# Kernel tuning notes

Measured on AMD Instinct MI355X. Metric: run time of the kernel, lower is better.

The kernel has to match this reference:

```python
import jax, jax.numpy as jnp
import numpy as np

BS, C_IN, CTX, TGT = 2, 8, 1024, 96
D_MODEL, N_HEADS, D_FF, N_LAYERS = 256, 16, 1024, 4
PF, SF, PC, SC = 8, 4, 32, 16
NF = (CTX + SF - PF) // SF + 1   # 256 fine patches (incl. end-pad)
NC = (CTX + SC - PC) // SC + 1   # 64 coarse patches
TOTAL = NF + NC                  # 320
EPS = 1e-5
DK = D_MODEL // N_HEADS
SCALE = DK ** -0.5


def _patchify(z, plen, stride):
    # ReplicationPad1d((0, stride)) then unfold -> (bs, c, n_patches, plen)
    pad = jnp.broadcast_to(z[..., -1:], z.shape[:-1] + (stride,))
    zp = jnp.concatenate([z, pad], axis=-1)
    n = (zp.shape[-1] - plen) // stride + 1
    idx = np.arange(n)[:, None] * stride + np.arange(plen)[None, :]
    return zp[..., idx]


def _layernorm(x, s, b):
    m = x.mean(-1, keepdims=True)
    v = jnp.var(x, axis=-1, keepdims=True)
    return (x - m) * jax.lax.rsqrt(v + EPS) * s + b


def setup_inputs() -> dict:
    key = jax.random.key(0)
    ks = jax.random.split(key, 16)
    g = lambda k, shape: jax.random.normal(k, shape, jnp.float32) * 0.02
    return {
        "z": jax.random.normal(ks[0], (BS, C_IN, CTX), jnp.float32),
        "revin_w": jnp.ones((C_IN,), jnp.float32),
        "revin_b": jnp.zeros((C_IN,), jnp.float32),
        "Wf": g(ks[1], (PF, D_MODEL)), "bf": jnp.zeros((D_MODEL,), jnp.float32),
        "Wc": g(ks[2], (PC, D_MODEL)), "bc": jnp.zeros((D_MODEL,), jnp.float32),
        "W_pos": jax.random.uniform(ks[3], (TOTAL, D_MODEL), jnp.float32, -0.02, 0.02),
        "WQ": g(ks[4], (N_LAYERS, D_MODEL, D_MODEL)), "bQ": jnp.zeros((N_LAYERS, D_MODEL), jnp.float32),
        "WK": g(ks[5], (N_LAYERS, D_MODEL, D_MODEL)), "bK": jnp.zeros((N_LAYERS, D_MODEL), jnp.float32),
        "WV": g(ks[6], (N_LAYERS, D_MODEL, D_MODEL)), "bV": jnp.zeros((N_LAYERS, D_MODEL), jnp.float32),
        "WO": g(ks[7], (N_LAYERS, D_MODEL, D_MODEL)), "bO": jnp.zeros((N_LAYERS, D_MODEL), jnp.float32),
        "ln1_s": jnp.ones((N_LAYERS, D_MODEL), jnp.float32), "ln1_b": jnp.zeros((N_LAYERS, D_MODEL), jnp.float32),
        "ln2_s": jnp.ones((N_LAYERS, D_MODEL), jnp.float32), "ln2_b": jnp.zeros((N_LAYERS, D_MODEL), jnp.float32),
        "F1": g(ks[8], (N_LAYERS, D_MODEL, D_FF)), "c1": jnp.zeros((N_LAYERS, D_FF), jnp.float32),
        "F2": g(ks[9], (N_LAYERS, D_FF, D_MODEL)), "c2": jnp.zeros((N_LAYERS, D_MODEL), jnp.float32),
        "Wh": g(ks[10], (D_MODEL * TOTAL, TGT)), "bh": jnp.zeros((TGT,), jnp.float32),
    }


def reference(z, revin_w, revin_b, Wf, bf, Wc, bc, W_pos, WQ, bQ, WK, bK, WV, bV,
              WO, bO, ln1_s, ln1_b, ln2_s, ln2_b, F1, c1, F2, c2, Wh, bh):
    # RevIN norm over the time axis (last axis of (bs, c, T))
    mean = z.mean(-1, keepdims=True)
    std = jnp.sqrt(jnp.var(z, axis=-1, keepdims=True) + EPS)
    zn = (z - mean) / std * revin_w[None, :, None] + revin_b[None, :, None]

    # dual-scale patch embedding
    x_fine = _patchify(zn, PF, SF) @ Wf + bf      # (bs, c, NF, d)
    x_coarse = _patchify(zn, PC, SC) @ Wc + bc    # (bs, c, NC, d)
    x = jnp.concatenate([x_fine, x_coarse], axis=2)  # (bs, c, TOTAL, d)

    u = x.reshape(BS * C_IN, TOTAL, D_MODEL) + W_pos  # (B, S, d), B=bs*c

    # residual-score transformer encoder (post-norm)
    prev = None
    for l in range(N_LAYERS):
        q = (u @ WQ[l] + bQ[l]).reshape(-1, TOTAL, N_HEADS, DK).transpose(0, 2, 1, 3)
        k = (u @ WK[l] + bK[l]).reshape(-1, TOTAL, N_HEADS, DK).transpose(0, 2, 1, 3)
        v = (u @ WV[l] + bV[l]).reshape(-1, TOTAL, N_HEADS, DK).transpose(0, 2, 1, 3)
        s = jnp.einsum('bhqd,bhkd->bhqk', q, k) * SCALE
        if prev is not None:
            s = s + prev
        w = jax.nn.softmax(s, axis=-1)
        o = jnp.einsum('bhqk,bhkd->bhqd', w, v).transpose(0, 2, 1, 3).reshape(-1, TOTAL, D_MODEL)
        o = o @ WO[l] + bO[l]
        u = _layernorm(u + o, ln1_s[l], ln1_b[l])
        h = jax.nn.gelu(u @ F1[l] + c1[l], approximate=False) @ F2[l] + c2[l]
        u = _layernorm(u + h, ln2_s[l], ln2_b[l])
        prev = s

    # head: (bs, c, TOTAL, d) -> permute -> flatten(d, TOTAL) -> linear
    zz = u.reshape(BS, C_IN, TOTAL, D_MODEL).transpose(0, 1, 3, 2).reshape(BS, C_IN, D_MODEL * TOTAL)
    out = zz @ Wh + bh  # (bs, c, TGT)

    # RevIN denorm
    out = (out - revin_b[None, :, None]) / (revin_w[None, :, None] + EPS * EPS) * std + mean
    return out
```

## Files before the change

### kernel.cpp

```cpp
#include <hip/hip_runtime.h>
#include <math.h>

typedef unsigned short ushort;
typedef unsigned int uint;
typedef __attribute__((ext_vector_type(8))) short short8;
typedef __attribute__((ext_vector_type(4))) float f32x4;
typedef __attribute__((ext_vector_type(4))) ushort us4;

constexpr int BS = 2, C_IN = 8, CTX = 1024, TGT = 96;
constexpr int DM = 256, NH = 16, DFF = 1024, NL = 4;
constexpr int NF = 256, TOTAL = 320;
constexpr int NB = 16;
constexpr int DK = 16;
constexpr float EPS = 1e-5f;
constexpr float SCALE = 0.25f;
constexpr int KHEAD = DM * TOTAL;
constexpr int M = NB * TOTAL;

__device__ __forceinline__ ushort f2b(float x) {
    uint u = __float_as_uint(x);
    u += 0x7fff + ((u >> 16) & 1);
    return (ushort)(u >> 16);
}
__device__ __forceinline__ float bu2f(ushort x) { return __uint_as_float(((uint)x) << 16); }
__device__ __forceinline__ uint pack2(float a, float b) { return (uint)f2b(a) | ((uint)f2b(b) << 16); }

typedef __attribute__((address_space(3))) uint lds_u32;
typedef const __attribute__((address_space(1))) uint glb_u32;
__device__ __forceinline__ void ldst16(const void* g, void* l) {
    __builtin_amdgcn_global_load_lds((glb_u32*)g, (lds_u32*)l, 16, 0, 0);
}

#define PIPE_BARRIER() asm volatile("s_waitcnt vmcnt(0)\n\ts_barrier" ::: "memory")

__global__ __launch_bounds__(256) void k_prep(
        const float* __restrict__ WQ, const float* __restrict__ WK,
        const float* __restrict__ WV, const float* __restrict__ WO,
        const float* __restrict__ F1, const float* __restrict__ F2,
        const float* __restrict__ Wh,
        ushort* __restrict__ Wtqkv, ushort* __restrict__ WtO,
        ushort* __restrict__ Ft1, ushort* __restrict__ Ft2,
        ushort* __restrict__ WhT2,
        const float* __restrict__ z, const float* __restrict__ rw,
        const float* __restrict__ rb,
        const float* __restrict__ Wf, const float* __restrict__ bfv,
        const float* __restrict__ Wc, const float* __restrict__ bcv,
        const float* __restrict__ Wpos, ushort* __restrict__ u,
        const float* __restrict__ bhv, float* __restrict__ outp,
        float* __restrict__ scalef) {
    __shared__ __align__(16) ushort tile[64 * 98];
    __shared__ float szn[CTX];
    __shared__ float red1[4], red2[4];
    int i = blockIdx.x, tid = threadIdx.x;

    if (i < 768) {
        const float* src; ushort* dst; int lsrc, ldst_, r0, c0;
        if (i < 256) {
            int mat = i >> 4, l = mat >> 2, w = mat & 3;
            src = (w == 0 ? WQ : (w == 1 ? WK : (w == 2 ? WV : WO))) + l * 65536;
            dst = (w < 3) ? (Wtqkv + (size_t)l * 768 * 256 + w * 65536)
                          : (WtO + (size_t)l * 65536);
            lsrc = 256; ldst_ = 256; r0 = ((i >> 2) & 3) * 64; c0 = (i & 3) * 64;
        } else if (i < 512) {
            int j = i - 256, l = j >> 6, t = j & 63;
            src = F1 + (size_t)l * 262144; dst = Ft1 + (size_t)l * 262144;
            lsrc = 1024; ldst_ = 256; r0 = (t >> 4) * 64; c0 = (t & 15) * 64;
        } else {
            int j = i - 512, l = j >> 6, t = j & 63;
            src = F2 + (size_t)l * 262144; dst = Ft2 + (size_t)l * 262144;
            lsrc = 256; ldst_ = 1024; r0 = (t >> 2) * 64; c0 = (t & 3) * 64;
        }
#pragma unroll
        for (int it = 0; it < 4; it++) {
            int fid = it * 256 + tid;
            int fr = fid >> 4, fc = fid & 15;
            f32x4 v = *(const f32x4*)&src[(size_t)(r0 + fr) * lsrc + c0 + fc * 4];
            ushort* tr = &tile[fr * 66];
            tr[fc * 4 + 0] = f2b(v[0]); tr[fc * 4 + 1] = f2b(v[1]);
            tr[fc * 4 + 2] = f2b(v[2]); tr[fc * 4 + 3] = f2b(v[3]);
        }
        __syncthreads();
#pragma unroll
        for (int it = 0; it < 4; it++) {
            int sid = it * 256 + tid;
            int cr = sid >> 4, cc = sid & 15;
            us4 v = (us4){ tile[(cc * 4 + 0) * 66 + cr], tile[(cc * 4 + 1) * 66 + cr],
                           tile[(cc * 4 + 2) * 66 + cr], tile[(cc * 4 + 3) * 66 + cr] };
            *(us4*)&dst[(size_t)(c0 + cr) * ldst_ + r0 + cc * 4] = v;
        }
    } else if (i < 2048) {
        int j = i - 768;
        int pp = j >> 2, d0 = (j & 3) * 64;
#pragma unroll
        for (int it = 0; it < 6; it++) {
            int fid = it * 256 + tid;
            int fr = fid / 24, fc = fid % 24;
            f32x4 v = *(const f32x4*)&Wh[((size_t)(d0 + fr) * 320 + pp) * 96 + fc * 4];
            ushort* tr = &tile[fr * 98];
            tr[fc * 4 + 0] = f2b(v[0]); tr[fc * 4 + 1] = f2b(v[1]);
            tr[fc * 4 + 2] = f2b(v[2]); tr[fc * 4 + 3] = f2b(v[3]);
        }
        __syncthreads();
#pragma unroll
        for (int it = 0; it < 6; it++) {
            int sid = it * 256 + tid;
            int tr = sid >> 4, dc = sid & 15;
            us4 v = (us4){ tile[(dc * 4 + 0) * 98 + tr], tile[(dc * 4 + 1) * 98 + tr],
                           tile[(dc * 4 + 2) * 98 + tr], tile[(dc * 4 + 3) * 98 + tr] };
            *(us4*)&WhT2[(size_t)tr * KHEAD + pp * 256 + d0 + dc * 4] = v;
        }
    } else {
        int j = i - 2048;
        int bc = j / 80, pb = j % 80;
        int wave = tid >> 6, lane = tid & 63;
        f32x4 zv = *(const f32x4*)&z[bc * CTX + tid * 4];
        float s1 = zv[0] + zv[1] + zv[2] + zv[3];
        float s2 = zv[0] * zv[0] + zv[1] * zv[1] + zv[2] * zv[2] + zv[3] * zv[3];
#pragma unroll
        for (int off = 1; off < 64; off <<= 1) {
            s1 += __shfl_xor(s1, off);
            s2 += __shfl_xor(s2, off);
        }
        if (lane == 0) { red1[wave] = s1; red2[wave] = s2; }
        __syncthreads();
        s1 = red1[0] + red1[1] + red1[2] + red1[3];
        s2 = red2[0] + red2[1] + red2[2] + red2[3];
        float m = s1 * (1.0f / CTX);
        float var = s2 * (1.0f / CTX) - m * m;
        float sd = sqrtf(var + EPS);
        int c = bc & 7;
        float w = rw[c], bb = rb[c];
        float inv_sd_w = w / sd;
#pragma unroll
        for (int k = 0; k < 4; k++) szn[tid * 4 + k] = (zv[k] - m) * inv_sd_w + bb;
        if (pb == 0) {
            if (tid < TGT) outp[bc * TGT + tid] = (bhv[tid] - bb) / (w + EPS * EPS) * sd + m;
            if (tid == 0) scalef[bc] = sd / (w + EPS * EPS);
        }
        __syncthreads();
#pragma unroll
        for (int pi = 0; pi < 4; pi++) {
            int p = pb * 4 + pi, d = tid;
            float acc;
            if (p < NF) {
                acc = bfv[d];
                int base = p * 4;
#pragma unroll
                for (int q = 0; q < 8; q++)
                    acc += szn[min(base + q, CTX - 1)] * Wf[q * DM + d];
            } else {
                acc = bcv[d];
                int base = (p - NF) * 16;
#pragma unroll
                for (int q = 0; q < 32; q++)
                    acc += szn[min(base + q, CTX - 1)] * Wc[q * DM + d];
            }
            acc += Wpos[p * DM + d];
            u[((size_t)bc * TOTAL + p) * DM + d] = f2b(acc);
        }
    }
}

template <int GELU, int QKV>
__global__ __launch_bounds__(256) void k_gemm_mfma(const ushort* __restrict__ A,
                                                   const ushort* __restrict__ Wt,
                                                   const float* __restrict__ b0,
                                                   const float* __restrict__ b1,
                                                   const float* __restrict__ b2,
                                                   ushort* __restrict__ C,
                                                   ushort* __restrict__ C2,
                                                   int Mm, int N, int K) {
    __shared__ ushort As[2][64][32];
    __shared__ ushort Bs[2][64][32];
    int tid = threadIdx.x;
    int wave = tid >> 6, lane = tid & 63;
    int quad = lane >> 4, l16 = lane & 15;
    int m0 = blockIdx.y * 64, n0 = blockIdx.x * 64;

    f32x4 acc[4];
#pragma unroll
    for (int nt = 0; nt < 4; nt++) acc[nt] = (f32x4){0.f, 0.f, 0.f, 0.f};

    int srow = wave * 16 + (lane >> 2);
    int sc = (lane & 3) ^ ((srow >> 1) & 3);
    const ushort* Ag = &A[(size_t)(m0 + srow) * K + sc * 8];
    const ushort* Bg = &Wt[(size_t)(n0 + srow) * K + sc * 8];
    int rchunk = (quad ^ ((l16 >> 1) & 3)) * 8;

    ldst16(Ag, &As[0][wave * 16][0]);
    ldst16(Bg, &Bs[0][wave * 16][0]);
    PIPE_BARRIER();

    int nstep = K >> 5;
    int cur = 0;
    for (int t = 0; t < nstep; t++) {
        if (t + 1 < nstep) {
            ldst16(Ag + (t + 1) * 32, &As[cur ^ 1][wave * 16][0]);
            ldst16(Bg + (t + 1) * 32, &Bs[cur ^ 1][wave * 16][0]);
        }
        short8 af = *(const short8*)&As[cur][wave * 16 + l16][rchunk];
#pragma unroll
        for (int nt = 0; nt < 4; nt++) {
            short8 bf = *(const short8*)&Bs[cur][nt * 16 + l16][rchunk];
            acc[nt] = __builtin_amdgcn_mfma_f32_16x16x32_bf16(af, bf, acc[nt], 0, 0, 0);
        }
        PIPE_BARRIER();
        cur ^= 1;
    }
#pragma unroll
    for (int nt = 0; nt < 4; nt++) {
        int col = n0 + nt * 16 + l16;
        float bi;
        if (QKV) {
            int bs = (n0 + nt * 16) >> 8;
            const float* bp = bs == 0 ? b0 : (bs == 1 ? b1 : b2);
            bi = bp[col & 255];
        } else {
            bi = b0[col];
        }
#pragma unroll
        for (int r = 0; r < 4; r++) {
            int rowm = m0 + wave * 16 + quad * 4 + r;
            float vv = acc[nt][r] + bi;
            if (GELU) vv = vv * 0.5f * (1.0f + erff(vv * 0.70710678118f));
            if (QKV) {
                int bs = col >> 8;
                int c = col & 255, hh = c >> 4, d = c & 15;
                int bb = rowm / 320, j = rowm - bb * 320;
                size_t plane = (size_t)hh * (M * DK) + (size_t)bb * (TOTAL * DK);
                if (bs == 0) {
                    C[plane + (size_t)j * DK + d] = f2b(vv);
                } else if (bs == 1) {
                    int off = (((j >> 4) * 2 + (d >> 3)) * 16 + (j & 15)) * 8 + (d & 7);
                    C[(size_t)M * DM + plane + off] = f2b(vv);
                } else {
                    int off = ((j >> 5) * 4 + ((j & 15) >> 2)) * 128 +
                              (((j >> 4) & 1) << 2) + (j & 3) + d * 8;
                    C2[plane + off] = f2b(vv);
                }
            } else {
                C[(size_t)rowm * N + col] = f2b(vv);
            }
        }
    }
}

__global__ __launch_bounds__(256) void k_gemm_ln16(const ushort* __restrict__ A,
                                                   const ushort* __restrict__ Wt,
                                                   const float* __restrict__ bias,
                                                   const float* __restrict__ ls,
                                                   const float* __restrict__ lb,
                                                   ushort* __restrict__ u, int K) {
    __shared__ ushort As[2][16][32];
    __shared__ ushort Bs[2][256][32];
    __shared__ float ps1[16][4], ps2[16][4];
    int tid = threadIdx.x;
    int wave = tid >> 6, lane = tid & 63;
    int quad = lane >> 4, l16 = lane & 15;
    int m0 = blockIdx.x * 16;

    f32x4 acc[4];
#pragma unroll
    for (int nt = 0; nt < 4; nt++) acc[nt] = (f32x4){0.f, 0.f, 0.f, 0.f};

    int brow = wave * 16 + (lane >> 2);
    int bc_swz = (lane & 3) ^ ((brow >> 1) & 3);
    const ushort* Bg0 = &Wt[(size_t)brow * K + bc_swz * 8];
    int ar = lane >> 2;
    int ac = (lane & 3) ^ ((ar >> 1) & 3);
    const ushort* Ag = &A[(size_t)(m0 + ar) * K + ac * 8];
    int rchunk = (quad ^ ((l16 >> 1) & 3)) * 8;

    if (tid < 64) ldst16(Ag, &As[0][0][0]);
#pragma unroll
    for (int i = 0; i < 4; i++)
        ldst16(Bg0 + (size_t)i * 64 * K, &Bs[0][i * 64 + wave * 16][0]);
    PIPE_BARRIER();

    int nstep = K >> 5;
    int cur = 0;
    for (int t = 0; t < nstep; t++) {
        if (t + 1 < nstep) {
            if (tid < 64) ldst16(Ag + (t + 1) * 32, &As[cur ^ 1][0][0]);
#pragma unroll
            for (int i = 0; i < 4; i++)
                ldst16(Bg0 + (size_t)i * 64 * K + (t + 1) * 32, &Bs[cur ^ 1][i * 64 + wave * 16][0]);
        }
        short8 af = *(const short8*)&As[cur][l16][rchunk];
#pragma unroll
        for (int nt = 0; nt < 4; nt++) {
            short8 bf = *(const short8*)&Bs[cur][wave * 64 + nt * 16 + l16][rchunk];
            acc[nt] = __builtin_amdgcn_mfma_f32_16x16x32_bf16(af, bf, acc[nt], 0, 0, 0);
        }
        PIPE_BARRIER();
        cur ^= 1;
    }
    float xv[4][4];
#pragma unroll
    for (int r = 0; r < 4; r++) {
        int rowg = m0 + quad * 4 + r;
        float s1 = 0.f, s2 = 0.f;
#pragma unroll
        for (int nt = 0; nt < 4; nt++) {
            int col = wave * 64 + nt * 16 + l16;
            float x = acc[nt][r] + bias[col] + bu2f(u[(size_t)rowg * DM + col]);
            xv[r][nt] = x; s1 += x; s2 += x * x;
        }
        s1 += __shfl_xor(s1, 1); s2 += __shfl_xor(s2, 1);
        s1 += __shfl_xor(s1, 2); s2 += __shfl_xor(s2, 2);
        s1 += __shfl_xor(s1, 4); s2 += __shfl_xor(s2, 4);
        s1 += __shfl_xor(s1, 8); s2 += __shfl_xor(s2, 8);
        if (l16 == 0) { ps1[quad * 4 + r][wave] = s1; ps2[quad * 4 + r][wave] = s2; }
    }
    __syncthreads();
#pragma unroll
    for (int r = 0; r < 4; r++) {
        int rowl = quad * 4 + r, rowg = m0 + rowl;
        float s1 = ps1[rowl][0] + ps1[rowl][1] + ps1[rowl][2] + ps1[rowl][3];
        float s2 = ps2[rowl][0] + ps2[rowl][1] + ps2[rowl][2] + ps2[rowl][3];
        float m = s1 * (1.0f / DM);
        float var = s2 * (1.0f / DM) - m * m;
        float rs = rsqrtf(var + EPS);
#pragma unroll
        for (int nt = 0; nt < 4; nt++) {
            int col = wave * 64 + nt * 16 + l16;
            u[(size_t)rowg * DM + col] = f2b((xv[r][nt] - m) * rs * ls[col] + lb[col]);
        }
    }
}

__global__ __launch_bounds__(256, 3) void k_attn(const ushort* __restrict__ qk, const ushort* __restrict__ vm,
                                                 ushort* __restrict__ ao, int nj) {
    __shared__ __align__(16) ushort sh[25600];
    int bh = blockIdx.x, b = bh >> 4, h = bh & 15;
    int i0 = blockIdx.y * 64;
    int t = threadIdx.x, wave = t >> 6, lane = t & 63, quad = lane >> 4, l16 = lane & 15;
    const short8 zero8 = (short8){0, 0, 0, 0, 0, 0, 0, 0};
    size_t hplane = (size_t)h * (M * DK) + (size_t)b * (TOTAL * DK);

    int nchunks = (nj + 1) * 10;
    for (int c = wave; c < nchunks; c += 4) {
        int s = c / 10, cc = c - s * 10;
        const ushort* src = (s < nj)
            ? qk + (size_t)(2 * s + 1) * (M * DM) + hplane + cc * 512
            : vm + hplane + cc * 512;
        int dstbase = (s < nj ? s * 5120 : 20480) + cc * 512;
        ldst16(src + lane * 8, &sh[dstbase]);
    }
    short8 qfr[4] = { zero8, zero8, zero8, zero8 };
    int qrow = i0 + wave * 16 + l16;
#pragma unroll
    for (int jl = 0; jl < 4; jl++)
        if (jl < nj && quad < 2)
            qfr[jl] = *(const short8*)&qk[(size_t)(2 * jl) * (M * DM) + hplane +
                                          (size_t)qrow * DK + quad * 8];
    PIPE_BARRIER();

    f32x4 acc[20];
#pragma unroll
    for (int nt = 0; nt < 20; nt++) acc[nt] = (f32x4){0.f, 0.f, 0.f, 0.f};

    __builtin_amdgcn_s_setprio(1);
#pragma unroll
    for (int jl = 0; jl < 4; jl++) {
        if (jl < nj) {
            int kb = jl * 5120;
#pragma unroll
            for (int nt = 0; nt < 20; nt++) {
                short8 kf = *(const short8*)&sh[kb + ((nt * 2 + (quad & 1)) * 16 + l16) * 8];
                acc[nt] = __builtin_amdgcn_mfma_f32_16x16x32_bf16(kf, qfr[jl], acc[nt], 0, 0, 0);
            }
        }
    }
    __builtin_amdgcn_s_setprio(0);

    float mx = -1e30f;
#pragma unroll
    for (int nt = 0; nt < 20; nt++)
#pragma unroll
        for (int r = 0; r < 4; r++) { acc[nt][r] *= SCALE; mx = fmaxf(mx, acc[nt][r]); }
    mx = fmaxf(mx, __shfl_xor(mx, 16));
    mx = fmaxf(mx, __shfl_xor(mx, 32));
    float sum = 0.f;
#pragma unroll
    for (int nt = 0; nt < 20; nt++)
#pragma unroll
        for (int r = 0; r < 4; r++) { acc[nt][r] = __expf(acc[nt][r] - mx); sum += acc[nt][r]; }
    sum += __shfl_xor(sum, 16);
    sum += __shfl_xor(sum, 32);
    float inv = 1.f / sum;
#pragma unroll
    for (int nt = 0; nt < 20; nt++)
#pragma unroll
        for (int r = 0; r < 4; r++) acc[nt][r] *= inv;

    f32x4 oacc = (f32x4){0.f, 0.f, 0.f, 0.f};
    __builtin_amdgcn_s_setprio(1);
#pragma unroll
    for (int jt2 = 0; jt2 < 10; jt2++) {
        short8 vt = *(const short8*)&sh[20480 + ((jt2 * 4 + quad) * 16 + l16) * 8];
        union { short8 v; uint u[4]; } pf;
        pf.u[0] = pack2(acc[2 * jt2][0], acc[2 * jt2][1]);
        pf.u[1] = pack2(acc[2 * jt2][2], acc[2 * jt2][3]);
        pf.u[2] = pack2(acc[2 * jt2 + 1][0], acc[2 * jt2 + 1][1]);
        pf.u[3] = pack2(acc[2 * jt2 + 1][2], acc[2 * jt2 + 1][3]);
        oacc = __builtin_amdgcn_mfma_f32_16x16x32_bf16(vt, pf.v, oacc, 0, 0, 0);
    }
    __builtin_amdgcn_s_setprio(0);
    us4 ov4 = (us4){f2b(oacc[0]), f2b(oacc[1]), f2b(oacc[2]), f2b(oacc[3])};
    *(us4*)&ao[((size_t)b * TOTAL + i0 + wave * 16 + l16) * DM + h * DK + quad * 4] = ov4;
}

__global__ __launch_bounds__(256) void k_head(const ushort* __restrict__ u, const ushort* __restrict__ WhT2,
                                              const float* __restrict__ scalef, float* __restrict__ out) {
    int t0 = blockIdx.x * 16;
    int wave = threadIdx.x >> 6, lane = threadIdx.x & 63;
    int quad = lane >> 4, l16 = lane & 15;
    int chunk = blockIdx.y * 4 + wave;
    int kbeg = chunk * 1024;
    f32x4 acc = (f32x4){0.f, 0.f, 0.f, 0.f};
    const ushort* za = &u[(size_t)l16 * KHEAD + quad * 8];
    const ushort* wb = &WhT2[(size_t)(t0 + l16) * KHEAD + quad * 8];
#pragma unroll 4
    for (int k = kbeg; k < kbeg + 1024; k += 32) {
        short8 af = *(const short8*)&za[k];
        short8 bf = *(const short8*)&wb[k];
        acc = __builtin_amdgcn_mfma_f32_16x16x32_bf16(af, bf, acc, 0, 0, 0);
    }
#pragma unroll
    for (int r = 0; r < 4; r++) {
        int bcr = quad * 4 + r;
        atomicAdd(&out[bcr * TGT + t0 + l16], acc[r] * scalef[bcr]);
    }
}

extern "C" void kernel_launch(void* const* d_in, const int* in_sizes, int n_in,
                              void* d_out, int out_size, void* d_ws, size_t ws_size,
                              hipStream_t stream) {
    const float* z       = (const float*)d_in[0];
    const float* revin_w = (const float*)d_in[1];
    const float* revin_b = (const float*)d_in[2];
    const float* Wf      = (const float*)d_in[3];
    const float* bfv     = (const float*)d_in[4];
    const float* Wc      = (const float*)d_in[5];
    const float* bcv     = (const float*)d_in[6];
    const float* Wpos    = (const float*)d_in[7];
    const float* WQ      = (const float*)d_in[8];
    const float* bQ      = (const float*)d_in[9];
    const float* WK      = (const float*)d_in[10];
    const float* bK      = (const float*)d_in[11];
    const float* WV      = (const float*)d_in[12];
    const float* bV      = (const float*)d_in[13];
    const float* WO      = (const float*)d_in[14];
    const float* bO      = (const float*)d_in[15];
    const float* ln1s    = (const float*)d_in[16];
    const float* ln1b    = (const float*)d_in[17];
    const float* ln2s    = (const float*)d_in[18];
    const float* ln2b    = (const float*)d_in[19];
    const float* F1      = (const float*)d_in[20];
    const float* c1      = (const float*)d_in[21];
    const float* F2      = (const float*)d_in[22];
    const float* c2      = (const float*)d_in[23];
    const float* Wh      = (const float*)d_in[24];
    const float* bh      = (const float*)d_in[25];
    float* out = (float*)d_out;

    char* p = (char*)d_ws;
    float* scalef = (float*)p;   p += 16 * 4;
    p = (char*)(((size_t)p + 255) & ~255ull);
    ushort* u     = (ushort*)p;  p += (size_t)M * DM * 2;
    ushort* qkbuf = (ushort*)p;  p += (size_t)NL * 2 * M * DM * 2;
    ushort* vbuf  = (ushort*)p;  p += (size_t)M * DM * 2;
    ushort* ax    = (ushort*)p;  p += (size_t)M * DM * 2;
    ushort* hbuf  = (ushort*)p;  p += (size_t)M * DFF * 2;
    ushort* Wtqkv = (ushort*)p;  p += (size_t)NL * 768 * 256 * 2;
    ushort* WtO   = (ushort*)p;  p += (size_t)NL * 256 * 256 * 2;
    ushort* Ft1   = (ushort*)p;  p += (size_t)NL * 1024 * 256 * 2;
    ushort* Ft2   = (ushort*)p;  p += (size_t)NL * 256 * 1024 * 2;
    ushort* WhT2  = (ushort*)p;  p += (size_t)TGT * KHEAD * 2;

    k_prep<<<3328, 256, 0, stream>>>(WQ, WK, WV, WO, F1, F2, Wh,
                                     Wtqkv, WtO, Ft1, Ft2, WhT2,
                                     z, revin_w, revin_b,
                                     Wf, bfv, Wc, bcv, Wpos, u,
                                     bh, out, scalef);

    for (int l = 0; l < NL; l++) {
        k_gemm_mfma<0, 1><<<dim3(12, 80), 256, 0, stream>>>(
            u, Wtqkv + (size_t)l * 768 * 256, bQ + l * DM, bK + l * DM, bV + l * DM,
            qkbuf + (size_t)l * 2 * M * DM, vbuf, M, 768, 256);
        k_attn<<<dim3(NB * NH, 5), 256, 0, stream>>>(qkbuf, vbuf, ax, l + 1);
        k_gemm_ln16<<<M / 16, 256, 0, stream>>>(
            ax, WtO + (size_t)l * 65536, bO + l * DM, ln1s + l * DM, ln1b + l * DM, u, 256);
        k_gemm_mfma<1, 0><<<dim3(16, 80), 256, 0, stream>>>(
            u, Ft1 + (size_t)l * 262144, c1 + l * DFF, c1, c1, hbuf, hbuf, M, 1024, 256);
        k_gemm_ln16<<<M / 16, 256, 0, stream>>>(
            hbuf, Ft2 + (size_t)l * 262144, c2 + l * DM, ln2s + l * DM, ln2b + l * DM, u, 1024);
    }

    k_head<<<dim3(TGT / 16, 20), 256, 0, stream>>>(u, WhT2, scalef, out);
}
```

Baseline: 426.1 us.

## Fuse O-proj+LN1, FFN up/GELU/down and LN2 into one per-row-block kernel

Replaces three launches per layer (O-projection with LayerNorm, the FF1 GEMM with GELU, and FF2 with LayerNorm) with a single kernel. Each 16-row block keeps the normalized activations and the GELU intermediate in shared memory and loops over the four 256-wide FF chunks, so the hidden buffer never goes through global memory. The cost is that each block re-streams all of F1/F2 from global/L2 with only 16 rows of reuse, and the grid is limited to 320 blocks doing serial chunk loops.

```diff
diff --git a/kernel.cpp b/kernel.cpp
--- a/kernel.cpp
+++ b/kernel.cpp
@@ -245,72 +245,183 @@
     }
 }
 
-__global__ __launch_bounds__(256) void k_gemm_ln16(const ushort* __restrict__ A,
-                                                   const ushort* __restrict__ Wt,
-                                                   const float* __restrict__ bias,
-                                                   const float* __restrict__ ls,
-                                                   const float* __restrict__ lb,
-                                                   ushort* __restrict__ u, int K) {
+__global__ __launch_bounds__(256) void k_block(const ushort* __restrict__ ax,
+                                               const ushort* __restrict__ WtO,
+                                               const float* __restrict__ bO,
+                                               const float* __restrict__ ln1s,
+                                               const float* __restrict__ ln1b,
+                                               const ushort* __restrict__ F1t,
+                                               const ushort* __restrict__ F2t,
+                                               const float* __restrict__ c1v,
+                                               const float* __restrict__ c2v,
+                                               const float* __restrict__ ln2s,
+                                               const float* __restrict__ ln2b,
+                                               ushort* __restrict__ u) {
     __shared__ ushort As[2][16][32];
     __shared__ ushort Bs[2][256][32];
+    __shared__ __align__(16) ushort Au[16][264];
+    __shared__ __align__(16) ushort Hs[16][264];
     __shared__ float ps1[16][4], ps2[16][4];
     int tid = threadIdx.x;
     int wave = tid >> 6, lane = tid & 63;
     int quad = lane >> 4, l16 = lane & 15;
     int m0 = blockIdx.x * 16;
 
-    f32x4 acc[4];
-#pragma unroll
-    for (int nt = 0; nt < 4; nt++) acc[nt] = (f32x4){0.f, 0.f, 0.f, 0.f};
-
     int brow = wave * 16 + (lane >> 2);
-    int bc_swz = (lane & 3) ^ ((brow >> 1) & 3);
-    const ushort* Bg0 = &Wt[(size_t)brow * K + bc_swz * 8];
+    int bsw = (lane & 3) ^ ((brow >> 1) & 3);
     int ar = lane >> 2;
     int ac = (lane & 3) ^ ((ar >> 1) & 3);
-    const ushort* Ag = &A[(size_t)(m0 + ar) * K + ac * 8];
     int rchunk = (quad ^ ((l16 >> 1) & 3)) * 8;
 
-    if (tid < 64) ldst16(Ag, &As[0][0][0]);
-#pragma unroll
-    for (int i = 0; i < 4; i++)
-        ldst16(Bg0 + (size_t)i * 64 * K, &Bs[0][i * 64 + wave * 16][0]);
-    PIPE_BARRIER();
-
-    int nstep = K >> 5;
-    int cur = 0;
-    for (int t = 0; t < nstep; t++) {
-        if (t + 1 < nstep) {
-            if (tid < 64) ldst16(Ag + (t + 1) * 32, &As[cur ^ 1][0][0]);
-#pragma unroll
-            for (int i = 0; i < 4; i++)
-                ldst16(Bg0 + (size_t)i * 64 * K + (t + 1) * 32, &Bs[cur ^ 1][i * 64 + wave * 16][0]);
-        }
-        short8 af = *(const short8*)&As[cur][l16][rchunk];
+    {
+        f32x4 acc[4];
+#pragma unroll
+        for (int nt = 0; nt < 4; nt++) acc[nt] = (f32x4){0.f, 0.f, 0.f, 0.f};
+        const ushort* Ag = &ax[(size_t)(m0 + ar) * 256 + ac * 8];
+        const ushort* Bg = &WtO[(size_t)brow * 256 + bsw * 8];
+
+        if (tid < 64) ldst16(Ag, &As[0][0][0]);
+#pragma unroll
+        for (int i = 0; i < 4; i++) ldst16(Bg + (size_t)i * 64 * 256, &Bs[0][i * 64 + wave * 16][0]);
+        PIPE_BARRIER();
+        int cur = 0;
+        for (int t = 0; t < 8; t++) {
+            if (t + 1 < 8) {
+                if (tid < 64) ldst16(Ag + (t + 1) * 32, &As[cur ^ 1][0][0]);
+#pragma unroll
+                for (int i = 0; i < 4; i++)
+                    ldst16(Bg + (size_t)i * 64 * 256 + (t + 1) * 32, &Bs[cur ^ 1][i * 64 + wave * 16][0]);
+            }
+            short8 af = *(const short8*)&As[cur][l16][rchunk];
+#pragma unroll
+            for (int nt = 0; nt < 4; nt++) {
+                short8 bf = *(const short8*)&Bs[cur][wave * 64 + nt * 16 + l16][rchunk];
+                acc[nt] = __builtin_amdgcn_mfma_f32_16x16x32_bf16(af, bf, acc[nt], 0, 0, 0);
+            }
+            PIPE_BARRIER();
+            cur ^= 1;
+        }
+        float xv[4][4];
+#pragma unroll
+        for (int r = 0; r < 4; r++) {
+            int rowg = m0 + quad * 4 + r;
+            float s1 = 0.f, s2 = 0.f;
+#pragma unroll
+            for (int nt = 0; nt < 4; nt++) {
+                int col = wave * 64 + nt * 16 + l16;
+                float x = acc[nt][r] + bO[col] + bu2f(u[(size_t)rowg * DM + col]);
+                xv[r][nt] = x; s1 += x; s2 += x * x;
+            }
+            s1 += __shfl_xor(s1, 1); s2 += __shfl_xor(s2, 1);
+            s1 += __shfl_xor(s1, 2); s2 += __shfl_xor(s2, 2);
+            s1 += __shfl_xor(s1, 4); s2 += __shfl_xor(s2, 4);
+            s1 += __shfl_xor(s1, 8); s2 += __shfl_xor(s2, 8);
+            if (l16 == 0) { ps1[quad * 4 + r][wave] = s1; ps2[quad * 4 + r][wave] = s2; }
+        }
+        __syncthreads();
+#pragma unroll
+        for (int r = 0; r < 4; r++) {
+            int rowl = quad * 4 + r;
+            float s1 = ps1[rowl][0] + ps1[rowl][1] + ps1[rowl][2] + ps1[rowl][3];
+            float s2 = ps2[rowl][0] + ps2[rowl][1] + ps2[rowl][2] + ps2[rowl][3];
+            float m = s1 * (1.0f / DM);
+            float var = s2 * (1.0f / DM) - m * m;
+            float rs = rsqrtf(var + EPS);
+#pragma unroll
+            for (int nt = 0; nt < 4; nt++) {
+                int col = wave * 64 + nt * 16 + l16;
+                int k32 = col >> 5, pp = (col >> 3) & 3, e = col & 7;
+                int pphys = pp ^ ((rowl >> 1) & 3);
+                Au[rowl][k32 * 32 + pphys * 8 + e] =
+                    f2b((xv[r][nt] - m) * rs * ln1s[col] + ln1b[col]);
+            }
+        }
+        __syncthreads();
+    }
+
+    f32x4 acc2[4];
+#pragma unroll
+    for (int nt = 0; nt < 4; nt++) acc2[nt] = (f32x4){0.f, 0.f, 0.f, 0.f};
+
+    for (int c = 0; c < 4; c++) {
+        f32x4 acc1[4];
+#pragma unroll
+        for (int nt = 0; nt < 4; nt++) acc1[nt] = (f32x4){0.f, 0.f, 0.f, 0.f};
+        const ushort* Bg1 = &F1t[(size_t)(c * 256 + brow) * 256 + bsw * 8];
+#pragma unroll
+        for (int i = 0; i < 4; i++) ldst16(Bg1 + (size_t)i * 64 * 256, &Bs[0][i * 64 + wave * 16][0]);
+        PIPE_BARRIER();
+        int cur = 0;
+        for (int t = 0; t < 8; t++) {
+            if (t + 1 < 8) {
+#pragma unroll
+                for (int i = 0; i < 4; i++)
+                    ldst16(Bg1 + (size_t)i * 64 * 256 + (t + 1) * 32, &Bs[cur ^ 1][i * 64 + wave * 16][0]);
+            }
+            short8 af = *(const short8*)&Au[l16][t * 32 + rchunk];
+#pragma unroll
+            for (int nt = 0; nt < 4; nt++) {
+                short8 bf = *(const short8*)&Bs[cur][wave * 64 + nt * 16 + l16][rchunk];
+                acc1[nt] = __builtin_amdgcn_mfma_f32_16x16x32_bf16(af, bf, acc1[nt], 0, 0, 0);
+            }
+            PIPE_BARRIER();
+            cur ^= 1;
+        }
 #pragma unroll
         for (int nt = 0; nt < 4; nt++) {
-            short8 bf = *(const short8*)&Bs[cur][wave * 64 + nt * 16 + l16][rchunk];
-            acc[nt] = __builtin_amdgcn_mfma_f32_16x16x32_bf16(af, bf, acc[nt], 0, 0, 0);
-        }
+            int cc = wave * 64 + nt * 16 + l16;
+            float bi = c1v[c * 256 + cc];
+            int k32 = cc >> 5, pp = (cc >> 3) & 3, e = cc & 7;
+#pragma unroll
+            for (int r = 0; r < 4; r++) {
+                int row = quad * 4 + r;
+                float vv = acc1[nt][r] + bi;
+                vv = vv * 0.5f * (1.0f + erff(vv * 0.70710678118f));
+                int pphys = pp ^ ((row >> 1) & 3);
+                Hs[row][k32 * 32 + pphys * 8 + e] = f2b(vv);
+            }
+        }
+        __syncthreads();
+        const ushort* Bg2 = &F2t[(size_t)brow * 1024 + c * 256 + bsw * 8];
+#pragma unroll
+        for (int i = 0; i < 4; i++) ldst16(Bg2 + (size_t)i * 64 * 1024, &Bs[0][i * 64 + wave * 16][0]);
         PIPE_BARRIER();
-        cur ^= 1;
-    }
+        cur = 0;
+        for (int t = 0; t < 8; t++) {
+            if (t + 1 < 8) {
+#pragma unroll
+                for (int i = 0; i < 4; i++)
+                    ldst16(Bg2 + (size_t)i * 64 * 1024 + (t + 1) * 32, &Bs[cur ^ 1][i * 64 + wave * 16][0]);
+            }
+            short8 af = *(const short8*)&Hs[l16][t * 32 + rchunk];
+#pragma unroll
+            for (int nt = 0; nt < 4; nt++) {
+                short8 bf = *(const short8*)&Bs[cur][wave * 64 + nt * 16 + l16][rchunk];
+                acc2[nt] = __builtin_amdgcn_mfma_f32_16x16x32_bf16(af, bf, acc2[nt], 0, 0, 0);
+            }
+            PIPE_BARRIER();
+            cur ^= 1;
+        }
+    }
+
     float xv[4][4];
 #pragma unroll
     for (int r = 0; r < 4; r++) {
-        int rowg = m0 + quad * 4 + r;
+        int rowl = quad * 4 + r;
         float s1 = 0.f, s2 = 0.f;
 #pragma unroll
         for (int nt = 0; nt < 4; nt++) {
             int col = wave * 64 + nt * 16 + l16;
-            float x = acc[nt][r] + bias[col] + bu2f(u[(size_t)rowg * DM + col]);
+            int k32 = col >> 5, pp = (col >> 3) & 3, e = col & 7;
+            int pphys = pp ^ ((rowl >> 1) & 3);
+            float x = acc2[nt][r] + c2v[col] + bu2f(Au[rowl][k32 * 32 + pphys * 8 + e]);
             xv[r][nt] = x; s1 += x; s2 += x * x;
         }
         s1 += __shfl_xor(s1, 1); s2 += __shfl_xor(s2, 1);
         s1 += __shfl_xor(s1, 2); s2 += __shfl_xor(s2, 2);
         s1 += __shfl_xor(s1, 4); s2 += __shfl_xor(s2, 4);
         s1 += __shfl_xor(s1, 8); s2 += __shfl_xor(s2, 8);
-        if (l16 == 0) { ps1[quad * 4 + r][wave] = s1; ps2[quad * 4 + r][wave] = s2; }
+        if (l16 == 0) { ps1[rowl][wave] = s1; ps2[rowl][wave] = s2; }
     }
     __syncthreads();
 #pragma unroll
@@ -324,7 +435,7 @@
 #pragma unroll
         for (int nt = 0; nt < 4; nt++) {
             int col = wave * 64 + nt * 16 + l16;
-            u[(size_t)rowg * DM + col] = f2b((xv[r][nt] - m) * rs * ls[col] + lb[col]);
+            u[(size_t)rowg * DM + col] = f2b((xv[r][nt] - m) * rs * ln2s[col] + ln2b[col]);
         }
     }
 }
@@ -472,7 +583,6 @@
     ushort* qkbuf = (ushort*)p;  p += (size_t)NL * 2 * M * DM * 2;
     ushort* vbuf  = (ushort*)p;  p += (size_t)M * DM * 2;
     ushort* ax    = (ushort*)p;  p += (size_t)M * DM * 2;
-    ushort* hbuf  = (ushort*)p;  p += (size_t)M * DFF * 2;
     ushort* Wtqkv = (ushort*)p;  p += (size_t)NL * 768 * 256 * 2;
     ushort* WtO   = (ushort*)p;  p += (size_t)NL * 256 * 256 * 2;
     ushort* Ft1   = (ushort*)p;  p += (size_t)NL * 1024 * 256 * 2;
@@ -490,12 +600,10 @@
             u, Wtqkv + (size_t)l * 768 * 256, bQ + l * DM, bK + l * DM, bV + l * DM,
             qkbuf + (size_t)l * 2 * M * DM, vbuf, M, 768, 256);
         k_attn<<<dim3(NB * NH, 5), 256, 0, stream>>>(qkbuf, vbuf, ax, l + 1);
-        k_gemm_ln16<<<M / 16, 256, 0, stream>>>(
-            ax, WtO + (size_t)l * 65536, bO + l * DM, ln1s + l * DM, ln1b + l * DM, u, 256);
-        k_gemm_mfma<1, 0><<<dim3(16, 80), 256, 0, stream>>>(
-            u, Ft1 + (size_t)l * 262144, c1 + l * DFF, c1, c1, hbuf, hbuf, M, 1024, 256);
-        k_gemm_ln16<<<M / 16, 256, 0, stream>>>(
-            hbuf, Ft2 + (size_t)l * 262144, c2 + l * DM, ln2s + l * DM, ln2b + l * DM, u, 1024);
+        k_block<<<M / 16, 256, 0, stream>>>(
+            ax, WtO + (size_t)l * 65536, bO + l * DM, ln1s + l * DM, ln1b + l * DM,
+            Ft1 + (size_t)l * 262144, Ft2 + (size_t)l * 262144,
+            c1 + l * DFF, c2 + l * DM, ln2s + l * DM, ln2b + l * DM, u);
     }
 
     k_head<<<dim3(TGT / 16, 20), 256, 0, stream>>>(u, WhT2, scalef, out);
```

After: 419.2 us. About the same (-1.6%).

## Use 128x128-tile GEMM for FFN with split-K partials and separate LN reduction

Applied to the files above, without the earlier changes.

Adds a 128x128 tiled MFMA GEMM used for FF1 with a fused GELU epilogue, and for FF2 as a 4-way split-K that writes fp32 partials. A new kernel then sums the partials, adds bias and the residual, and applies LayerNorm. The 16-row GEMM+LN kernel for FF2 is dropped, which aims to raise tile reuse and parallelism for the K=1024 GEMM. In exchange, the partial buffer costs extra fp32 global traffic and one more kernel launch per layer, and a second u buffer is added so the residual is read separately from the output.

```diff
diff --git a/kernel.cpp b/kernel.cpp
--- a/kernel.cpp
+++ b/kernel.cpp
@@ -245,12 +245,94 @@
     }
 }
 
+template <int GELU, int PART>
+__global__ __launch_bounds__(256) void k_gemm128(const ushort* __restrict__ A,
+                                                 const ushort* __restrict__ Wt,
+                                                 const float* __restrict__ bias,
+                                                 ushort* __restrict__ C,
+                                                 float* __restrict__ Cp,
+                                                 int N, int K, int kc) {
+    __shared__ ushort As[2][128][32];
+    __shared__ ushort Bs[2][128][32];
+    int tid = threadIdx.x;
+    int wave = tid >> 6, lane = tid & 63;
+    int quad = lane >> 4, l16 = lane & 15;
+    int wr = wave >> 1, wc = wave & 1;
+    int m0 = blockIdx.y * 128, n0 = blockIdx.x * 128;
+    int kbeg = blockIdx.z * kc;
+
+    f32x4 acc[4][4];
+#pragma unroll
+    for (int mi = 0; mi < 4; mi++)
+#pragma unroll
+        for (int ni = 0; ni < 4; ni++) acc[mi][ni] = (f32x4){0.f, 0.f, 0.f, 0.f};
+
+    int r4 = lane >> 2;
+    int sc = (lane & 3) ^ ((r4 >> 1) & 3);
+    int srow0 = wave * 32 + r4, srow1 = wave * 32 + 16 + r4;
+    const ushort* Ag0 = &A[(size_t)(m0 + srow0) * K + kbeg + sc * 8];
+    const ushort* Ag1 = &A[(size_t)(m0 + srow1) * K + kbeg + sc * 8];
+    const ushort* Bg0 = &Wt[(size_t)(n0 + srow0) * K + kbeg + sc * 8];
+    const ushort* Bg1 = &Wt[(size_t)(n0 + srow1) * K + kbeg + sc * 8];
+    int rchunk = (quad ^ ((l16 >> 1) & 3)) * 8;
+
+    ldst16(Ag0, &As[0][wave * 32][0]);
+    ldst16(Ag1, &As[0][wave * 32 + 16][0]);
+    ldst16(Bg0, &Bs[0][wave * 32][0]);
+    ldst16(Bg1, &Bs[0][wave * 32 + 16][0]);
+    PIPE_BARRIER();
+
+    int nstep = kc >> 5;
+    int cur = 0;
+    for (int t = 0; t < nstep; t++) {
+        if (t + 1 < nstep) {
+            ldst16(Ag0 + (t + 1) * 32, &As[cur ^ 1][wave * 32][0]);
+            ldst16(Ag1 + (t + 1) * 32, &As[cur ^ 1][wave * 32 + 16][0]);
+            ldst16(Bg0 + (t + 1) * 32, &Bs[cur ^ 1][wave * 32][0]);
+            ldst16(Bg1 + (t + 1) * 32, &Bs[cur ^ 1][wave * 32 + 16][0]);
+        }
+        short8 af[4], bf[4];
+#pragma unroll
+        for (int mi = 0; mi < 4; mi++)
+            af[mi] = *(const short8*)&As[cur][wr * 64 + mi * 16 + l16][rchunk];
+#pragma unroll
+        for (int ni = 0; ni < 4; ni++)
+            bf[ni] = *(const short8*)&Bs[cur][wc * 64 + ni * 16 + l16][rchunk];
+#pragma unroll
+        for (int mi = 0; mi < 4; mi++)
+#pragma unroll
+            for (int ni = 0; ni < 4; ni++)
+                acc[mi][ni] = __builtin_amdgcn_mfma_f32_16x16x32_bf16(af[mi], bf[ni], acc[mi][ni], 0, 0, 0);
+        PIPE_BARRIER();
+        cur ^= 1;
+    }
+
+#pragma unroll
+    for (int mi = 0; mi < 4; mi++)
+#pragma unroll
+        for (int ni = 0; ni < 4; ni++) {
+            int col = n0 + wc * 64 + ni * 16 + l16;
+#pragma unroll
+            for (int r = 0; r < 4; r++) {
+                int row = m0 + wr * 64 + mi * 16 + quad * 4 + r;
+                if (PART) {
+                    Cp[((size_t)blockIdx.z * M + row) * N + col] = acc[mi][ni][r];
+                } else {
+                    float vv = acc[mi][ni][r] + bias[col];
+                    if (GELU) vv = vv * 0.5f * (1.0f + erff(vv * 0.70710678118f));
+                    C[(size_t)row * N + col] = f2b(vv);
+                }
+            }
+        }
+}
+
 __global__ __launch_bounds__(256) void k_gemm_ln16(const ushort* __restrict__ A,
                                                    const ushort* __restrict__ Wt,
                                                    const float* __restrict__ bias,
                                                    const float* __restrict__ ls,
                                                    const float* __restrict__ lb,
-                                                   ushort* __restrict__ u, int K) {
+                                                   const ushort* __restrict__ ures,
+                                                   ushort* __restrict__ uout, int K) {
     __shared__ ushort As[2][16][32];
     __shared__ ushort Bs[2][256][32];
     __shared__ float ps1[16][4], ps2[16][4];
@@ -303,7 +385,7 @@
 #pragma unroll
         for (int nt = 0; nt < 4; nt++) {
             int col = wave * 64 + nt * 16 + l16;
-            float x = acc[nt][r] + bias[col] + bu2f(u[(size_t)rowg * DM + col]);
+            float x = acc[nt][r] + bias[col] + bu2f(ures[(size_t)rowg * DM + col]);
             xv[r][nt] = x; s1 += x; s2 += x * x;
         }
         s1 += __shfl_xor(s1, 1); s2 += __shfl_xor(s2, 1);
@@ -324,8 +406,48 @@
 #pragma unroll
         for (int nt = 0; nt < 4; nt++) {
             int col = wave * 64 + nt * 16 + l16;
-            u[(size_t)rowg * DM + col] = f2b((xv[r][nt] - m) * rs * ls[col] + lb[col]);
-        }
+            uout[(size_t)rowg * DM + col] = f2b((xv[r][nt] - m) * rs * ls[col] + lb[col]);
+        }
+    }
+}
+
+__global__ __launch_bounds__(256) void k_ln2red4(const float* __restrict__ part,
+                                                 const float* __restrict__ c2v,
+                                                 const ushort* __restrict__ u1,
+                                                 const float* __restrict__ ls,
+                                                 const float* __restrict__ lb,
+                                                 ushort* __restrict__ u) {
+    int tid = threadIdx.x;
+    int wave = tid >> 6, lane = tid & 63;
+    int m0 = blockIdx.x * 16;
+#pragma unroll
+    for (int r = 0; r < 4; r++) {
+        int row = m0 + wave * 4 + r;
+        f32x4 a = *(const f32x4*)&part[(size_t)row * 256 + lane * 4];
+        f32x4 b = *(const f32x4*)&part[((size_t)M + row) * 256 + lane * 4];
+        f32x4 c = *(const f32x4*)&part[((size_t)2 * M + row) * 256 + lane * 4];
+        f32x4 d = *(const f32x4*)&part[((size_t)3 * M + row) * 256 + lane * 4];
+        us4 ur = *(const us4*)&u1[(size_t)row * 256 + lane * 4];
+        float x[4];
+        float s1 = 0.f, s2 = 0.f;
+#pragma unroll
+        for (int j = 0; j < 4; j++) {
+            x[j] = a[j] + b[j] + c[j] + d[j] + c2v[lane * 4 + j] + bu2f(ur[j]);
+            s1 += x[j]; s2 += x[j] * x[j];
+        }
+#pragma unroll
+        for (int off = 1; off < 64; off <<= 1) {
+            s1 += __shfl_xor(s1, off);
+            s2 += __shfl_xor(s2, off);
+        }
+        float m = s1 * (1.0f / DM);
+        float var = s2 * (1.0f / DM) - m * m;
+        float rs = rsqrtf(var + EPS);
+        us4 o;
+#pragma unroll
+        for (int j = 0; j < 4; j++)
+            o[j] = f2b((x[j] - m) * rs * ls[lane * 4 + j] + lb[lane * 4 + j]);
+        *(us4*)&u[(size_t)row * 256 + lane * 4] = o;
     }
 }
 
@@ -469,10 +591,12 @@
     float* scalef = (float*)p;   p += 16 * 4;
     p = (char*)(((size_t)p + 255) & ~255ull);
     ushort* u     = (ushort*)p;  p += (size_t)M * DM * 2;
+    ushort* u1    = (ushort*)p;  p += (size_t)M * DM * 2;
     ushort* qkbuf = (ushort*)p;  p += (size_t)NL * 2 * M * DM * 2;
     ushort* vbuf  = (ushort*)p;  p += (size_t)M * DM * 2;
     ushort* ax    = (ushort*)p;  p += (size_t)M * DM * 2;
     ushort* hbuf  = (ushort*)p;  p += (size_t)M * DFF * 2;
+    float* part   = (float*)p;   p += (size_t)4 * M * 256 * 4;
     ushort* Wtqkv = (ushort*)p;  p += (size_t)NL * 768 * 256 * 2;
     ushort* WtO   = (ushort*)p;  p += (size_t)NL * 256 * 256 * 2;
     ushort* Ft1   = (ushort*)p;  p += (size_t)NL * 1024 * 256 * 2;
@@ -491,11 +615,14 @@
             qkbuf + (size_t)l * 2 * M * DM, vbuf, M, 768, 256);
         k_attn<<<dim3(NB * NH, 5), 256, 0, stream>>>(qkbuf, vbuf, ax, l + 1);
         k_gemm_ln16<<<M / 16, 256, 0, stream>>>(
-            ax, WtO + (size_t)l * 65536, bO + l * DM, ln1s + l * DM, ln1b + l * DM, u, 256);
-        k_gemm_mfma<1, 0><<<dim3(16, 80), 256, 0, stream>>>(
-            u, Ft1 + (size_t)l * 262144, c1 + l * DFF, c1, c1, hbuf, hbuf, M, 1024, 256);
-        k_gemm_ln16<<<M / 16, 256, 0, stream>>>(
-            hbuf, Ft2 + (size_t)l * 262144, c2 + l * DM, ln2s + l * DM, ln2b + l * DM, u, 1024);
+            ax, WtO + (size_t)l * 65536, bO + l * DM, ln1s + l * DM, ln1b + l * DM,
+            u, u1, 256);
+        k_gemm128<1, 0><<<dim3(8, 40, 1), 256, 0, stream>>>(
+            u1, Ft1 + (size_t)l * 262144, c1 + l * DFF, hbuf, nullptr, 1024, 256, 256);
+        k_gemm128<0, 1><<<dim3(2, 40, 4), 256, 0, stream>>>(
+            hbuf, Ft2 + (size_t)l * 262144, nullptr, nullptr, part, 256, 1024, 256);
+        k_ln2red4<<<M / 16, 256, 0, stream>>>(
+            part, c2 + l * DM, u1, ln2s + l * DM, ln2b + l * DM, u);
     }
 
     k_head<<<dim3(TGT / 16, 20), 256, 0, stream>>>(u, WhT2, scalef, out);
```

New measurement: 423.7 us. About the same (-0.6%).
